# Kernel tuning notes

Measured on AMD Instinct MI355X. Metric: run time of the kernel, lower is better.

## Reference

```python
import jax, jax.numpy as jnp
import numpy as np

N = 3072
D = 256
H = 8
HD = D // H
E = 98304
NUM_EDGE_TYPES = 16
MAX_DIST = 10
MAX_DEG = 512
BIAS_SCALE = 10.0
ATTN_TEMP = 0.5
EPS = 1e-5


def _ln(x, g, b):
    m = x.mean(-1, keepdims=True)
    v = ((x - m) ** 2).mean(-1, keepdims=True)
    return (x - m) / jnp.sqrt(v + EPS) * g + b


def setup_inputs() -> dict:
    key = jax.random.key(0)
    ks = jax.random.split(key, 24)
    f32 = jnp.float32
    x = jax.random.normal(ks[0], (N, D), f32)
    edge_index = jax.random.randint(ks[1], (2, E), 0, N)
    edge_types = jax.random.randint(ks[2], (E,), 0, NUM_EDGE_TYPES)
    pos_encoding = jax.random.uniform(ks[3], (N, N), f32)
    edge_weights = jax.random.uniform(ks[4], (E,), f32)
    s = 0.02
    Wq = jax.random.normal(ks[5], (D, D), f32) * s
    Wk = jax.random.normal(ks[6], (D, D), f32) * s
    Wv = jax.random.normal(ks[7], (D, D), f32) * s
    Wo = jax.random.normal(ks[8], (D, D), f32) * s
    bq = jnp.zeros((D,), f32); bk = jnp.zeros((D,), f32)
    bv = jnp.zeros((D,), f32); bo = jnp.zeros((D,), f32)
    spd_table = jax.random.normal(ks[9], (MAX_DIST + 2, H), f32) * s
    edge_type_table = jax.random.normal(ks[10], (NUM_EDGE_TYPES, H), f32) * s
    self_loop_bias = jnp.ones((H,), f32)
    in_deg_emb = jax.random.normal(ks[11], (MAX_DEG + 1, D), f32) * s
    out_deg_emb = jax.random.normal(ks[12], (MAX_DEG + 1, D), f32) * s
    degree_scale = jnp.ones((1,), f32)
    ln1_g = jnp.ones((D,), f32); ln1_b = jnp.zeros((D,), f32)
    ln2_g = jnp.ones((D,), f32); ln2_b = jnp.zeros((D,), f32)
    W1 = jax.random.normal(ks[13], (D, 4 * D), f32) * s
    b1 = jnp.zeros((4 * D,), f32)
    W2 = jax.random.normal(ks[14], (4 * D, D), f32) * s
    b2 = jnp.zeros((D,), f32)
    return dict(x=x, edge_index=edge_index, edge_types=edge_types,
                pos_encoding=pos_encoding, edge_weights=edge_weights,
                Wq=Wq, bq=bq, Wk=Wk, bk=bk, Wv=Wv, bv=bv, Wo=Wo, bo=bo,
                spd_table=spd_table, edge_type_table=edge_type_table,
                self_loop_bias=self_loop_bias, in_deg_emb=in_deg_emb,
                out_deg_emb=out_deg_emb, degree_scale=degree_scale,
                ln1_g=ln1_g, ln1_b=ln1_b, ln2_g=ln2_g, ln2_b=ln2_b,
                W1=W1, b1=b1, W2=W2, b2=b2)


def reference(x, edge_index, edge_types, pos_encoding, edge_weights,
              Wq, bq, Wk, bk, Wv, bv, Wo, bo,
              spd_table, edge_type_table, self_loop_bias,
              in_deg_emb, out_deg_emb, degree_scale,
              ln1_g, ln1_b, ln2_g, ln2_b, W1, b1, W2, b2):
    src, dst = edge_index[0], edge_index[1]
    ones = jnp.ones((E,), jnp.int32)
    deg_out = jnp.clip(jax.ops.segment_sum(ones, src, num_segments=N), 0, MAX_DEG)
    deg_in = jnp.clip(jax.ops.segment_sum(ones, dst, num_segments=N), 0, MAX_DEG)
    x = x + (in_deg_emb[deg_in] + out_deg_emb[deg_out]) * degree_scale
    xn = _ln(x, ln1_g, ln1_b)
    q = (xn @ Wq + bq).reshape(N, H, HD).transpose(1, 0, 2)  # [H,N,hd]
    k = (xn @ Wk + bk).reshape(N, H, HD).transpose(1, 0, 2)
    v = (xn @ Wv + bv).reshape(N, H, HD).transpose(1, 0, 2)
    # structural attention bias [H,N,N]
    spd = pos_encoding[:, :N]
    bucket = jnp.where(spd == 0, 0,
             jnp.where(spd > 1.0, MAX_DIST + 1,
                       jnp.clip(spd * MAX_DIST, 1, MAX_DIST).astype(jnp.int32)))
    bias = spd_table[bucket].transpose(2, 0, 1) * BIAS_SCALE
    bias = bias + self_loop_bias[:, None, None] * jnp.eye(N, dtype=bias.dtype)
    e_bias = edge_type_table[edge_types] + edge_weights[:, None] * (2.0 * BIAS_SCALE)  # [E,H]
    bias = bias.at[:, src, dst].add((e_bias * BIAS_SCALE).T)
    # SDPA path: q/temp, k/temp then 1/sqrt(hd) scale -> 1/(temp^2*sqrt(hd))
    scale = 1.0 / (ATTN_TEMP * ATTN_TEMP * np.sqrt(HD).astype(np.float32))
    scores = jnp.einsum('hnd,hmd->hnm', q, k) * scale + bias
    attn = jax.nn.softmax(scores, axis=-1)
    attn_out = jnp.einsum('hnm,hmd->hnd', attn, v).transpose(1, 0, 2).reshape(N, D)
    x = x + attn_out @ Wo + bo
    y = _ln(x, ln2_g, ln2_b)
    y = jax.nn.gelu(y @ W1 + b1, approximate=False) @ W2 + b2
    return x + y
```

## Files before the change

kernel.cpp:

```cpp
#include <hip/hip_runtime.h>
#include <hip/hip_bf16.h>

#define NN 3072
#define DM 256
#define NH 8
#define HDIM 32
#define NE 98304
#define DFF 1024
#define MAXDEG 512
#define NIT 192
#define NJT 48
#define JSPLIT 2

typedef short bf16x8 __attribute__((ext_vector_type(8)));
typedef float f32x4 __attribute__((ext_vector_type(4)));
typedef unsigned short u16;
typedef unsigned int u32;

#define MFMA16 __builtin_amdgcn_mfma_f32_16x16x32_bf16

__device__ __forceinline__ u16 f2bf(float f){
  u32 u = __builtin_bit_cast(u32, f);
  u32 r = (u + 0x7FFFu + ((u >> 16) & 1u)) >> 16;
  return (u16)r;
}

__global__ void k_deg(const int* __restrict__ src, const int* __restrict__ dst,
                      int* __restrict__ deg_out, int* __restrict__ deg_in,
                      int* __restrict__ bcnt){
  int e = blockIdx.x * 256 + threadIdx.x;
  if (e < NE){
    int s = src[e], d = dst[e];
    atomicAdd(&deg_out[s], 1);
    atomicAdd(&deg_in[d], 1);
    atomicAdd(&bcnt[(s >> 4) * NJT + (d >> 6)], 1);
  }
}

__global__ __launch_bounds__(1024)
void k_scan(const int* __restrict__ cnt, int* __restrict__ ptr){
  __shared__ int sc[1024];
  int t = threadIdx.x;
  int loc[9]; int s = 0;
  #pragma unroll
  for (int u = 0; u < 9; u++){ loc[u] = cnt[t*9 + u]; s += loc[u]; }
  sc[t] = s;
  __syncthreads();
  for (int off = 1; off < 1024; off <<= 1){
    int v = (t >= off) ? sc[t-off] : 0;
    __syncthreads();
    sc[t] += v;
    __syncthreads();
  }
  int run = sc[t] - s;
  #pragma unroll
  for (int u = 0; u < 9; u++){ ptr[t*9 + u] = run; run += loc[u]; }
  if (t == 1023) ptr[9216] = run;
}

__global__ void k_scatter(const int* __restrict__ src, const int* __restrict__ dst,
                          const int* __restrict__ types, const float* __restrict__ w,
                          const int* __restrict__ bptr, int* __restrict__ bfill,
                          u16* __restrict__ meta, float* __restrict__ ews){
  int e = blockIdx.x * 256 + threadIdx.x;
  if (e < NE){
    int s = src[e], d = dst[e];
    int b = (s >> 4) * NJT + (d >> 6);
    int slot = bptr[b] + atomicAdd(&bfill[b], 1);
    meta[slot] = (u16)((s & 15) | ((d & 63) << 4) | (types[e] << 10));
    ews[slot] = w[e];
  }
}

__global__ __launch_bounds__(1024)
void k_bucket(const float* __restrict__ pos, unsigned char* __restrict__ bktP){
  int j = blockIdx.x * 1024 + threadIdx.x;
  int i = blockIdx.y;
  float spv = pos[(size_t)i*NN + j];
  int bkt;
  if (spv == 0.f) bkt = 0;
  else if (spv > 1.f) bkt = 11;
  else { float cc = fminf(fmaxf(spv * 10.f, 1.f), 10.f); bkt = (int)cc; }
  bktP[(size_t)i*NN + (j & ~63) + (j & 15)*4 + ((j >> 4) & 3)] = (unsigned char)bkt;
}

__global__ __launch_bounds__(256)
void k_trans(const float* __restrict__ Wq, const float* __restrict__ Wk,
             const float* __restrict__ Wv, const float* __restrict__ Wo,
             const float* __restrict__ W1, const float* __restrict__ W2,
             u16* __restrict__ Wqkvot, u16* __restrict__ W1t, u16* __restrict__ W2t){
  __shared__ u16 t_[32][33];
  int bt = blockIdx.x;
  const float* srcm; u16* dstm; int K, N, kt, nt;
  if (bt < 256){
    int m = bt >> 6, r = bt & 63; kt = r >> 3; nt = r & 7; K = 256; N = 256;
    srcm = (m==0)?Wq:(m==1)?Wk:(m==2)?Wv:Wo; dstm = Wqkvot + m*65536;
  } else if (bt < 512){
    int r = bt - 256; kt = r >> 5; nt = r & 31; K = 256; N = 1024; srcm = W1; dstm = W1t;
  } else {
    int r = bt - 512; kt = r >> 3; nt = r & 7; K = 1024; N = 256; srcm = W2; dstm = W2t;
  }
  int tx = threadIdx.x & 31, ty = threadIdx.x >> 5;
  #pragma unroll
  for (int s = 0; s < 4; s++)
    t_[ty + 8*s][tx] = f2bf(srcm[(size_t)(kt*32 + ty + 8*s)*N + nt*32 + tx]);
  __syncthreads();
  #pragma unroll
  for (int s = 0; s < 4; s++)
    dstm[(size_t)(nt*32 + ty + 8*s)*K + kt*32 + tx] = t_[tx][ty + 8*s];
}

__global__ __launch_bounds__(256)
void k_ln(const float* __restrict__ in, const int* __restrict__ deg_in,
          const int* __restrict__ deg_out, const float* __restrict__ in_emb,
          const float* __restrict__ out_emb, const float* __restrict__ dscale,
          const float* __restrict__ g, const float* __restrict__ b,
          float* __restrict__ save_f32, u16* __restrict__ out_bf){
  int i = blockIdx.x, c = threadIdx.x;
  size_t idx = (size_t)i*DM + c;
  float val = in[idx];
  if (deg_in){
    int di = min(deg_in[i], MAXDEG), dg = min(deg_out[i], MAXDEG);
    val += (in_emb[(size_t)di*DM + c] + out_emb[(size_t)dg*DM + c]) * dscale[0];
    save_f32[idx] = val;
  }
  float s = val, s2 = val*val;
  #pragma unroll
  for (int off = 32; off; off >>= 1){
    s  += __shfl_xor(s, off);
    s2 += __shfl_xor(s2, off);
  }
  __shared__ float red[8];
  int lane = c & 63, w = c >> 6;
  if (lane == 0){ red[w] = s; red[4+w] = s2; }
  __syncthreads();
  s  = red[0] + red[1] + red[2] + red[3];
  s2 = red[4] + red[5] + red[6] + red[7];
  float mean = s * (1.f/256.f);
  float var = s2 * (1.f/256.f) - mean*mean;
  float xn = (val - mean) * rsqrtf(var + 1e-5f) * g[c] + b[c];
  out_bf[idx] = f2bf(xn);
}

__global__ __launch_bounds__(256)
void k_gemm(const u16* __restrict__ A, const u16* __restrict__ Bt,
            const float* __restrict__ b0, const float* __restrict__ b1,
            const float* __restrict__ b2, const float* __restrict__ res,
            void* __restrict__ out, void* __restrict__ out2,
            int K, int Ncols, int mode){
  __shared__ u16 sA[64][40];
  __shared__ u16 sB[64][40];
  const int tid = threadIdx.x, lane = tid & 63, wid = tid >> 6;
  const int m0 = blockIdx.y * 64, n0 = blockIdx.x * 64;
  const int wr = (wid >> 1) * 32, wc = (wid & 1) * 32;
  const int srow = tid >> 2, scol = (tid & 3) * 8;
  const int fr = lane & 15, fg = lane >> 4;
  f32x4 acc00 = {0,0,0,0}, acc01 = {0,0,0,0}, acc10 = {0,0,0,0}, acc11 = {0,0,0,0};
  for (int k0 = 0; k0 < K; k0 += 32){
    __syncthreads();
    *(bf16x8*)&sA[srow][scol] = *(const bf16x8*)&A[(size_t)(m0+srow)*K + k0 + scol];
    *(bf16x8*)&sB[srow][scol] = *(const bf16x8*)&Bt[(size_t)(n0+srow)*K + k0 + scol];
    __syncthreads();
    bf16x8 a0 = *(const bf16x8*)&sA[wr + fr][fg*8];
    bf16x8 a1 = *(const bf16x8*)&sA[wr + 16 + fr][fg*8];
    bf16x8 b0f = *(const bf16x8*)&sB[wc + fr][fg*8];
    bf16x8 b1f = *(const bf16x8*)&sB[wc + 16 + fr][fg*8];
    acc00 = MFMA16(a0, b0f, acc00, 0, 0, 0);
    acc01 = MFMA16(a0, b1f, acc01, 0, 0, 0);
    acc10 = MFMA16(a1, b0f, acc10, 0, 0, 0);
    acc11 = MFMA16(a1, b1f, acc11, 0, 0, 0);
  }
  #pragma unroll
  for (int fm = 0; fm < 2; fm++)
  #pragma unroll
  for (int fn = 0; fn < 2; fn++){
    f32x4 c = (fm==0) ? ((fn==0) ? acc00 : acc01) : ((fn==0) ? acc10 : acc11);
    #pragma unroll
    for (int r = 0; r < 4; r++){
      int row = m0 + wr + fm*16 + fg*4 + r;
      int col = n0 + wc + fn*16 + fr;
      if (mode == 5){
        int seg = col >> 8, cn = col & 255;
        const float* bp = (seg==0) ? b0 : (seg==1) ? b1 : b2;
        float val = c[r] + bp[cn];
        if (seg < 2) ((u16*)out)[(size_t)seg*NN*DM + (size_t)row*DM + cn] = f2bf(val);
        else         ((u16*)out2)[(size_t)cn*NN + row] = f2bf(val);
      } else {
        float val = c[r] + b0[col];
        size_t idx = (size_t)row*Ncols + col;
        if (mode == 2) ((float*)out)[idx] = res[idx] + val;
        else           ((u16*)out)[idx] = f2bf(0.5f*val*(1.f + erff(val*0.70710678f)));
      }
    }
  }
}

__global__ __launch_bounds__(512)
void k_attn(const u16* __restrict__ qb, const u16* __restrict__ kb, const u16* __restrict__ vT,
            const unsigned char* __restrict__ bktP,
            const float* __restrict__ spd_table, const float* __restrict__ slb,
            const u16* __restrict__ meta, const float* __restrict__ ews,
            const float* __restrict__ ett, const int* __restrict__ bptr,
            float* __restrict__ opart, float* __restrict__ mpart, float* __restrict__ lpart){
  __shared__ float s_spd[96];
  __shared__ float s_ett[128];
  __shared__ float s_sc[NH][16][68];
  const int tid = threadIdx.x, lane = tid & 63, h = tid >> 6;
  const int it = blockIdx.x, jc = blockIdx.y;
  const int i0 = it * 16;
  const float SCALE = 0.70710678f;
  if (tid < 96) s_spd[tid] = spd_table[tid] * 10.f;
  else if (tid >= 128 && tid < 256) s_ett[tid-128] = ett[tid-128] * 10.f;
  const float slbh = slb[h];
  const int fr = lane & 15, fg = lane >> 4;
  bf16x8 qv = *(const bf16x8*)&qb[(size_t)(i0 + fr)*DM + h*HDIM + fg*8];
  float (*sc)[68] = s_sc[h];
  f32x4 o0 = {0,0,0,0}, o1 = {0,0,0,0};
  float m_run = -3.0e38f, l_run = 0.f;
  __syncthreads();

  for (int jt = jc*(NJT/JSPLIT); jt < (jc+1)*(NJT/JSPLIT); ++jt){
    const int j0 = jt * 64;
    bf16x8 kf0 = *(const bf16x8*)&kb[(size_t)(j0      + fr)*DM + h*HDIM + fg*8];
    bf16x8 kf1 = *(const bf16x8*)&kb[(size_t)(j0 + 16 + fr)*DM + h*HDIM + fg*8];
    bf16x8 kf2 = *(const bf16x8*)&kb[(size_t)(j0 + 32 + fr)*DM + h*HDIM + fg*8];
    bf16x8 kf3 = *(const bf16x8*)&kb[(size_t)(j0 + 48 + fr)*DM + h*HDIM + fg*8];
    uchar4 bk0 = *(const uchar4*)&bktP[(size_t)(i0 + fg*4 + 0)*NN + j0 + fr*4];
    uchar4 bk1 = *(const uchar4*)&bktP[(size_t)(i0 + fg*4 + 1)*NN + j0 + fr*4];
    uchar4 bk2 = *(const uchar4*)&bktP[(size_t)(i0 + fg*4 + 2)*NN + j0 + fr*4];
    uchar4 bk3 = *(const uchar4*)&bktP[(size_t)(i0 + fg*4 + 3)*NN + j0 + fr*4];
    f32x4 z = {0,0,0,0};
    f32x4 s0 = MFMA16(qv, kf0, z, 0, 0, 0);
    f32x4 s1 = MFMA16(qv, kf1, z, 0, 0, 0);
    f32x4 s2 = MFMA16(qv, kf2, z, 0, 0, 0);
    f32x4 s3 = MFMA16(qv, kf3, z, 0, 0, 0);
    unsigned char bb[4][4] = {{bk0.x,bk0.y,bk0.z,bk0.w},{bk1.x,bk1.y,bk1.z,bk1.w},
                              {bk2.x,bk2.y,bk2.z,bk2.w},{bk3.x,bk3.y,bk3.z,bk3.w}};
    #pragma unroll
    for (int r = 0; r < 4; r++){
      int row = fg*4 + r;
      #pragma unroll
      for (int c2 = 0; c2 < 4; c2++){
        int col = c2*16 + fr;
        float sv = (c2==0) ? s0[r] : (c2==1) ? s1[r] : (c2==2) ? s2[r] : s3[r];
        float val = sv * SCALE + s_spd[(int)bb[r][c2]*8 + h];
        if (i0 + row == j0 + col) val += slbh;
        sc[row][col] = val;
      }
    }
    {
      int e0 = bptr[it*NJT + jt], e1 = bptr[it*NJT + jt + 1];
      for (int ix = e0 + lane; ix < e1; ix += 64){
        u16 me = meta[ix];
        int il = me & 15, jl = (me >> 4) & 63, tp = me >> 10;
        atomicAdd(&sc[il][jl], s_ett[tp*8 + h] + 200.f * ews[ix]);
      }
    }
    float v[16];
    { f32x4 a = *(const f32x4*)&sc[fr][fg*8];
      v[0]=a[0]; v[1]=a[1]; v[2]=a[2]; v[3]=a[3]; }
    { f32x4 a = *(const f32x4*)&sc[fr][fg*8 + 4];
      v[4]=a[0]; v[5]=a[1]; v[6]=a[2]; v[7]=a[3]; }
    { f32x4 a = *(const f32x4*)&sc[fr][32 + fg*8];
      v[8]=a[0]; v[9]=a[1]; v[10]=a[2]; v[11]=a[3]; }
    { f32x4 a = *(const f32x4*)&sc[fr][32 + fg*8 + 4];
      v[12]=a[0]; v[13]=a[1]; v[14]=a[2]; v[15]=a[3]; }
    float mx = v[0];
    #pragma unroll
    for (int t = 1; t < 16; t++) mx = fmaxf(mx, v[t]);
    mx = fmaxf(mx, __shfl_xor(mx, 16));
    mx = fmaxf(mx, __shfl_xor(mx, 32));
    float mnew = fmaxf(m_run, mx);
    float fac = __expf(m_run - mnew);
    float p[16], ps = 0.f;
    #pragma unroll
    for (int t = 0; t < 16; t++){ p[t] = __expf(v[t] - mnew); ps += p[t]; }
    ps += __shfl_xor(ps, 16);
    ps += __shfl_xor(ps, 32);
    l_run = l_run * fac + ps;
    m_run = mnew;
    float f0 = __shfl(fac, fg*4 + 0);
    float f1 = __shfl(fac, fg*4 + 1);
    float f2 = __shfl(fac, fg*4 + 2);
    float f3 = __shfl(fac, fg*4 + 3);
    o0[0]*=f0; o0[1]*=f1; o0[2]*=f2; o0[3]*=f3;
    o1[0]*=f0; o1[1]*=f1; o1[2]*=f2; o1[3]*=f3;
    union { u16 a[8]; bf16x8 v8; } pa0u, pa1u;
    #pragma unroll
    for (int t = 0; t < 8; t++){ pa0u.a[t] = f2bf(p[t]); pa1u.a[t] = f2bf(p[8+t]); }
    bf16x8 vf00 = *(const bf16x8*)&vT[(size_t)(h*HDIM      + fr)*NN + j0      + fg*8];
    bf16x8 vf01 = *(const bf16x8*)&vT[(size_t)(h*HDIM      + fr)*NN + j0 + 32 + fg*8];
    bf16x8 vf10 = *(const bf16x8*)&vT[(size_t)(h*HDIM + 16 + fr)*NN + j0      + fg*8];
    bf16x8 vf11 = *(const bf16x8*)&vT[(size_t)(h*HDIM + 16 + fr)*NN + j0 + 32 + fg*8];
    o0 = MFMA16(pa0u.v8, vf00, o0, 0, 0, 0);
    o0 = MFMA16(pa1u.v8, vf01, o0, 0, 0, 0);
    o1 = MFMA16(pa0u.v8, vf10, o1, 0, 0, 0);
    o1 = MFMA16(pa1u.v8, vf11, o1, 0, 0, 0);
  }

  float* ob = opart + (size_t)jc*NN*DM;
  #pragma unroll
  for (int r = 0; r < 4; r++){
    size_t row = i0 + fg*4 + r;
    ob[row*DM + h*HDIM + fr]      = o0[r];
    ob[row*DM + h*HDIM + 16 + fr] = o1[r];
  }
  if (fg == 0){
    mpart[jc*NN*NH + (i0 + fr)*NH + h] = m_run;
    lpart[jc*NN*NH + (i0 + fr)*NH + h] = l_run;
  }
}

__global__ __launch_bounds__(256)
void k_reduce(const float* __restrict__ opart, const float* __restrict__ mpart,
              const float* __restrict__ lpart, u16* __restrict__ aob){
  int row = blockIdx.x, col = threadIdx.x, h = col >> 5;
  float m0 = mpart[row*NH + h], m1 = mpart[NN*NH + row*NH + h];
  float l0 = lpart[row*NH + h], l1 = lpart[NN*NH + row*NH + h];
  float M = fmaxf(m0, m1);
  float w0 = __expf(m0 - M), w1 = __expf(m1 - M);
  float L = l0*w0 + l1*w1;
  float a = opart[(size_t)row*DM + col], b = opart[(size_t)NN*DM + (size_t)row*DM + col];
  aob[(size_t)row*DM + col] = f2bf((a*w0 + b*w1) / L);
}

extern "C" void kernel_launch(void* const* d_in, const int* in_sizes, int n_in,
                              void* d_out, int out_size, void* d_ws, size_t ws_size,
                              hipStream_t stream){
  const float* x     = (const float*)d_in[0];
  const int*   ei    = (const int*)d_in[1];
  const int*   etyp  = (const int*)d_in[2];
  const float* pos   = (const float*)d_in[3];
  const float* ewin  = (const float*)d_in[4];
  const float* Wq    = (const float*)d_in[5];
  const float* bq    = (const float*)d_in[6];
  const float* Wk    = (const float*)d_in[7];
  const float* bk    = (const float*)d_in[8];
  const float* Wv    = (const float*)d_in[9];
  const float* bv    = (const float*)d_in[10];
  const float* Wo    = (const float*)d_in[11];
  const float* bo    = (const float*)d_in[12];
  const float* spd   = (const float*)d_in[13];
  const float* ett   = (const float*)d_in[14];
  const float* slb   = (const float*)d_in[15];
  const float* inde  = (const float*)d_in[16];
  const float* outde = (const float*)d_in[17];
  const float* dsc   = (const float*)d_in[18];
  const float* ln1g  = (const float*)d_in[19];
  const float* ln1b  = (const float*)d_in[20];
  const float* ln2g  = (const float*)d_in[21];
  const float* ln2b  = (const float*)d_in[22];
  const float* W1    = (const float*)d_in[23];
  const float* b1    = (const float*)d_in[24];
  const float* W2    = (const float*)d_in[25];
  const float* b2    = (const float*)d_in[26];
  const int* src = ei;
  const int* dst = ei + NE;

  char* p = (char*)d_ws;
  auto alloc = [&](size_t bytes) -> void* {
    void* r = (void*)p;
    p += (bytes + 255) & ~(size_t)255;
    return r;
  };
  int*  deg_in  = (int*)alloc(NN*4);
  int*  deg_out = (int*)alloc(NN*4);
  int*  bcnt    = (int*)alloc(9216*4);
  int*  bfill   = (int*)alloc(9216*4);
  int*  bptr    = (int*)alloc(9217*4);
  u16*  meta    = (u16*)alloc(NE*2);
  float* ews    = (float*)alloc(NE*4);
  unsigned char* bktP = (unsigned char*)alloc((size_t)NN*NN);
  float* xb     = (float*)alloc((size_t)NN*DM*4);
  float* x2     = (float*)alloc((size_t)NN*DM*4);
  u16*  xnb     = (u16*)alloc((size_t)NN*DM*2);
  u16*  x2nb    = (u16*)alloc((size_t)NN*DM*2);
  u16*  qb      = (u16*)alloc((size_t)NN*DM*2);
  u16*  kb      = (u16*)alloc((size_t)NN*DM*2);
  u16*  vT      = (u16*)alloc((size_t)NN*DM*2);
  u16*  aob     = (u16*)alloc((size_t)NN*DM*2);
  u16*  h1b     = (u16*)alloc((size_t)NN*DFF*2);
  float* opart  = (float*)alloc((size_t)JSPLIT*NN*DM*4);
  float* mpart  = (float*)alloc((size_t)JSPLIT*NN*NH*4);
  float* lpart  = (float*)alloc((size_t)JSPLIT*NN*NH*4);
  u16*  Wqkvot  = (u16*)alloc(4*65536*2);
  u16*  W1t     = (u16*)alloc(262144*2);
  u16*  W2t     = (u16*)alloc(262144*2);
  (void)kb;

  hipMemsetAsync(deg_in, 0, (2*NN + 2*9216)*4, stream);

  k_deg<<<NE/256, 256, 0, stream>>>(src, dst, deg_out, deg_in, bcnt);
  k_scan<<<1, 1024, 0, stream>>>(bcnt, bptr);
  k_scatter<<<NE/256, 256, 0, stream>>>(src, dst, etyp, ewin, bptr, bfill, meta, ews);
  k_bucket<<<dim3(3, NN), 1024, 0, stream>>>(pos, bktP);
  k_trans<<<768, 256, 0, stream>>>(Wq, Wk, Wv, Wo, W1, W2, Wqkvot, W1t, W2t);
  k_ln<<<NN, 256, 0, stream>>>(x, deg_in, deg_out, inde, outde, dsc, ln1g, ln1b, xb, xnb);

  k_gemm<<<dim3(12, 48), 256, 0, stream>>>(xnb, Wqkvot, bq, bk, bv, nullptr,
                                           qb, vT, DM, 768, 5);

  k_attn<<<dim3(NIT, JSPLIT), 512, 0, stream>>>(qb, kb, vT, bktP, spd, slb, meta, ews,
                                                ett, bptr, opart, mpart, lpart);
  k_reduce<<<NN, 256, 0, stream>>>(opart, mpart, lpart, aob);

  u16* Wot = Wqkvot + 3*65536;
  k_gemm<<<dim3(4, 48), 256, 0, stream>>>(aob, Wot, bo, nullptr, nullptr, xb,
                                          x2, nullptr, DM, DM, 2);
  k_ln<<<NN, 256, 0, stream>>>(x2, nullptr, nullptr, nullptr, nullptr, nullptr,
                               ln2g, ln2b, nullptr, x2nb);
  k_gemm<<<dim3(16, 48), 256, 0, stream>>>(x2nb, W1t, b1, nullptr, nullptr, nullptr,
                                           h1b, nullptr, DM, DFF, 3);
  k_gemm<<<dim3(4, 48), 256, 0, stream>>>(h1b, W2t, b2, nullptr, nullptr, x2,
                                          d_out, nullptr, DFF, DM, 2);
}
```

Baseline: 327.8 us.

## Split attention keys four ways, widen GEMM K-step, fold Q scale, pack bf16 converts

Attention now splits the key range into four chunks instead of two, which raises block count and occupancy, and the reduce kernel is generalised to combine any number of chunks. The GEMM stages 64-wide K tiles to halve the number of barriers per output tile. The softmax scale is folded into Q at projection time, the bias tables are re-laid-out per head, and the diagonal check is limited to the diagonal tile. P is converted to bf16 with packed conversion instructions. In exchange the partial buffers and reduce traffic double. The removed __syncthreads relies on each wave filling its own table slice, and reads of Q scaled before rounding to bf16 change precision slightly.

```diff
diff --git a/kernel.cpp b/kernel.cpp
--- a/kernel.cpp
+++ b/kernel.cpp
@@ -10,7 +10,7 @@
 #define MAXDEG 512
 #define NIT 192
 #define NJT 48
-#define JSPLIT 2
+#define JSPLIT 4
 
 typedef short bf16x8 __attribute__((ext_vector_type(8)));
 typedef float f32x4 __attribute__((ext_vector_type(4)));
@@ -23,6 +23,9 @@
   u32 u = __builtin_bit_cast(u32, f);
   u32 r = (u + 0x7FFFu + ((u >> 16) & 1u)) >> 16;
   return (u16)r;
+}
+__device__ __forceinline__ u32 cvtpk(float lo, float hi){
+  u32 r; asm("v_cvt_pk_bf16_f32 %0, %1, %2" : "=v"(r) : "v"(lo), "v"(hi)); return r;
 }
 
 __global__ void k_deg(const int* __restrict__ src, const int* __restrict__ dst,
@@ -148,27 +151,32 @@
             const float* __restrict__ b2, const float* __restrict__ res,
             void* __restrict__ out, void* __restrict__ out2,
             int K, int Ncols, int mode){
-  __shared__ u16 sA[64][40];
-  __shared__ u16 sB[64][40];
+  __shared__ u16 sA[64][72];
+  __shared__ u16 sB[64][72];
   const int tid = threadIdx.x, lane = tid & 63, wid = tid >> 6;
   const int m0 = blockIdx.y * 64, n0 = blockIdx.x * 64;
   const int wr = (wid >> 1) * 32, wc = (wid & 1) * 32;
-  const int srow = tid >> 2, scol = (tid & 3) * 8;
+  const int srow = tid >> 2, scol = (tid & 3) * 16;
   const int fr = lane & 15, fg = lane >> 4;
   f32x4 acc00 = {0,0,0,0}, acc01 = {0,0,0,0}, acc10 = {0,0,0,0}, acc11 = {0,0,0,0};
-  for (int k0 = 0; k0 < K; k0 += 32){
+  for (int k0 = 0; k0 < K; k0 += 64){
     __syncthreads();
-    *(bf16x8*)&sA[srow][scol] = *(const bf16x8*)&A[(size_t)(m0+srow)*K + k0 + scol];
-    *(bf16x8*)&sB[srow][scol] = *(const bf16x8*)&Bt[(size_t)(n0+srow)*K + k0 + scol];
+    *(bf16x8*)&sA[srow][scol]     = *(const bf16x8*)&A[(size_t)(m0+srow)*K + k0 + scol];
+    *(bf16x8*)&sA[srow][scol + 8] = *(const bf16x8*)&A[(size_t)(m0+srow)*K + k0 + scol + 8];
+    *(bf16x8*)&sB[srow][scol]     = *(const bf16x8*)&Bt[(size_t)(n0+srow)*K + k0 + scol];
+    *(bf16x8*)&sB[srow][scol + 8] = *(const bf16x8*)&Bt[(size_t)(n0+srow)*K + k0 + scol + 8];
     __syncthreads();
-    bf16x8 a0 = *(const bf16x8*)&sA[wr + fr][fg*8];
-    bf16x8 a1 = *(const bf16x8*)&sA[wr + 16 + fr][fg*8];
-    bf16x8 b0f = *(const bf16x8*)&sB[wc + fr][fg*8];
-    bf16x8 b1f = *(const bf16x8*)&sB[wc + 16 + fr][fg*8];
-    acc00 = MFMA16(a0, b0f, acc00, 0, 0, 0);
-    acc01 = MFMA16(a0, b1f, acc01, 0, 0, 0);
-    acc10 = MFMA16(a1, b0f, acc10, 0, 0, 0);
-    acc11 = MFMA16(a1, b1f, acc11, 0, 0, 0);
+    #pragma unroll
+    for (int kk = 0; kk < 2; kk++){
+      bf16x8 a0  = *(const bf16x8*)&sA[wr + fr][kk*32 + fg*8];
+      bf16x8 a1  = *(const bf16x8*)&sA[wr + 16 + fr][kk*32 + fg*8];
+      bf16x8 b0f = *(const bf16x8*)&sB[wc + fr][kk*32 + fg*8];
+      bf16x8 b1f = *(const bf16x8*)&sB[wc + 16 + fr][kk*32 + fg*8];
+      acc00 = MFMA16(a0, b0f, acc00, 0, 0, 0);
+      acc01 = MFMA16(a0, b1f, acc01, 0, 0, 0);
+      acc10 = MFMA16(a1, b0f, acc10, 0, 0, 0);
+      acc11 = MFMA16(a1, b1f, acc11, 0, 0, 0);
+    }
   }
   #pragma unroll
   for (int fm = 0; fm < 2; fm++)
@@ -183,6 +191,7 @@
         int seg = col >> 8, cn = col & 255;
         const float* bp = (seg==0) ? b0 : (seg==1) ? b1 : b2;
         float val = c[r] + bp[cn];
+        if (seg == 0) val *= 0.70710678f;
         if (seg < 2) ((u16*)out)[(size_t)seg*NN*DM + (size_t)row*DM + cn] = f2bf(val);
         else         ((u16*)out2)[(size_t)cn*NN + row] = f2bf(val);
       } else {
@@ -202,22 +211,20 @@
             const u16* __restrict__ meta, const float* __restrict__ ews,
             const float* __restrict__ ett, const int* __restrict__ bptr,
             float* __restrict__ opart, float* __restrict__ mpart, float* __restrict__ lpart){
-  __shared__ float s_spd[96];
-  __shared__ float s_ett[128];
   __shared__ float s_sc[NH][16][68];
+  __shared__ float s_spdw[NH][32];
+  __shared__ float s_ettw[NH][32];
   const int tid = threadIdx.x, lane = tid & 63, h = tid >> 6;
   const int it = blockIdx.x, jc = blockIdx.y;
   const int i0 = it * 16;
-  const float SCALE = 0.70710678f;
-  if (tid < 96) s_spd[tid] = spd_table[tid] * 10.f;
-  else if (tid >= 128 && tid < 256) s_ett[tid-128] = ett[tid-128] * 10.f;
+  if (lane < 12) s_spdw[h][lane] = spd_table[lane*8 + h] * 10.f;
+  if (lane < 16) s_ettw[h][lane] = ett[lane*8 + h] * 10.f;
   const float slbh = slb[h];
   const int fr = lane & 15, fg = lane >> 4;
   bf16x8 qv = *(const bf16x8*)&qb[(size_t)(i0 + fr)*DM + h*HDIM + fg*8];
   float (*sc)[68] = s_sc[h];
   f32x4 o0 = {0,0,0,0}, o1 = {0,0,0,0};
   float m_run = -3.0e38f, l_run = 0.f;
-  __syncthreads();
 
   for (int jt = jc*(NJT/JSPLIT); jt < (jc+1)*(NJT/JSPLIT); ++jt){
     const int j0 = jt * 64;
@@ -236,6 +243,7 @@
     f32x4 s3 = MFMA16(qv, kf3, z, 0, 0, 0);
     unsigned char bb[4][4] = {{bk0.x,bk0.y,bk0.z,bk0.w},{bk1.x,bk1.y,bk1.z,bk1.w},
                               {bk2.x,bk2.y,bk2.z,bk2.w},{bk3.x,bk3.y,bk3.z,bk3.w}};
+    const bool dg_tile = (j0 == (i0 & ~63));
     #pragma unroll
     for (int r = 0; r < 4; r++){
       int row = fg*4 + r;
@@ -243,8 +251,8 @@
       for (int c2 = 0; c2 < 4; c2++){
         int col = c2*16 + fr;
         float sv = (c2==0) ? s0[r] : (c2==1) ? s1[r] : (c2==2) ? s2[r] : s3[r];
-        float val = sv * SCALE + s_spd[(int)bb[r][c2]*8 + h];
-        if (i0 + row == j0 + col) val += slbh;
+        float val = sv + s_spdw[h][(int)bb[r][c2]];
+        if (dg_tile && (i0 + row == j0 + col)) val += slbh;
         sc[row][col] = val;
       }
     }
@@ -253,7 +261,7 @@
       for (int ix = e0 + lane; ix < e1; ix += 64){
         u16 me = meta[ix];
         int il = me & 15, jl = (me >> 4) & 63, tp = me >> 10;
-        atomicAdd(&sc[il][jl], s_ett[tp*8 + h] + 200.f * ews[ix]);
+        atomicAdd(&sc[il][jl], s_ettw[h][tp] + 200.f * ews[ix]);
       }
     }
     float v[16];
@@ -285,9 +293,12 @@
     float f3 = __shfl(fac, fg*4 + 3);
     o0[0]*=f0; o0[1]*=f1; o0[2]*=f2; o0[3]*=f3;
     o1[0]*=f0; o1[1]*=f1; o1[2]*=f2; o1[3]*=f3;
-    union { u16 a[8]; bf16x8 v8; } pa0u, pa1u;
-    #pragma unroll
-    for (int t = 0; t < 8; t++){ pa0u.a[t] = f2bf(p[t]); pa1u.a[t] = f2bf(p[8+t]); }
+    union { u32 w[4]; bf16x8 v8; } pa0u, pa1u;
+    #pragma unroll
+    for (int t = 0; t < 4; t++){
+      pa0u.w[t] = cvtpk(p[2*t], p[2*t+1]);
+      pa1u.w[t] = cvtpk(p[8 + 2*t], p[9 + 2*t]);
+    }
     bf16x8 vf00 = *(const bf16x8*)&vT[(size_t)(h*HDIM      + fr)*NN + j0      + fg*8];
     bf16x8 vf01 = *(const bf16x8*)&vT[(size_t)(h*HDIM      + fr)*NN + j0 + 32 + fg*8];
     bf16x8 vf10 = *(const bf16x8*)&vT[(size_t)(h*HDIM + 16 + fr)*NN + j0      + fg*8];
@@ -315,13 +326,22 @@
 void k_reduce(const float* __restrict__ opart, const float* __restrict__ mpart,
               const float* __restrict__ lpart, u16* __restrict__ aob){
   int row = blockIdx.x, col = threadIdx.x, h = col >> 5;
-  float m0 = mpart[row*NH + h], m1 = mpart[NN*NH + row*NH + h];
-  float l0 = lpart[row*NH + h], l1 = lpart[NN*NH + row*NH + h];
-  float M = fmaxf(m0, m1);
-  float w0 = __expf(m0 - M), w1 = __expf(m1 - M);
-  float L = l0*w0 + l1*w1;
-  float a = opart[(size_t)row*DM + col], b = opart[(size_t)NN*DM + (size_t)row*DM + col];
-  aob[(size_t)row*DM + col] = f2bf((a*w0 + b*w1) / L);
+  float m[JSPLIT], l[JSPLIT];
+  float M = -3.0e38f;
+  #pragma unroll
+  for (int jc = 0; jc < JSPLIT; jc++){
+    m[jc] = mpart[jc*NN*NH + row*NH + h];
+    l[jc] = lpart[jc*NN*NH + row*NH + h];
+    M = fmaxf(M, m[jc]);
+  }
+  float L = 0.f, acc = 0.f;
+  #pragma unroll
+  for (int jc = 0; jc < JSPLIT; jc++){
+    float w = __expf(m[jc] - M);
+    L += l[jc] * w;
+    acc += opart[(size_t)jc*NN*DM + (size_t)row*DM + col] * w;
+  }
+  aob[(size_t)row*DM + col] = f2bf(acc / L);
 }
 
 extern "C" void kernel_launch(void* const* d_in, const int* in_sizes, int n_in,
@@ -386,7 +406,6 @@
   u16*  Wqkvot  = (u16*)alloc(4*65536*2);
   u16*  W1t     = (u16*)alloc(262144*2);
   u16*  W2t     = (u16*)alloc(262144*2);
-  (void)kb;
 
   hipMemsetAsync(deg_in, 0, (2*NN + 2*9216)*4, stream);
 
```

Result: faster. 313.9 us (-4.2%).
